# Kernel tuning notes

Hardware: AMD Instinct MI355X
Metric: run time of the kernel (lower is better)

The kernel has to match this reference:

```python
import jax, jax.numpy as jnp
import numpy as np


def _position_table(seq_len, d_model, dtype):
    # position[i, j] = sin(i / 10000**((j+1)/d))  if j even
    #                  cos(i / 10000**((j+1)/d))  if j odd
    # (note the nonstandard (j+1)/d exponent, faithful to the source)
    i = jnp.arange(seq_len, dtype=dtype)[:, None]          # [S, 1]
    j = jnp.arange(d_model, dtype=dtype)[None, :]          # [1, D]
    pf = i / jnp.power(jnp.asarray(10000.0, dtype), (j + 1.0) / d_model)  # [S, D]
    even = (jnp.arange(d_model) % 2 == 0)[None, :]
    return jnp.where(even, jnp.sin(pf), jnp.cos(pf))       # [S, D]


def setup_inputs() -> dict:
    key = jax.random.key(0)
    x = jax.random.normal(key, (4, 8192, 1024), dtype=jnp.float32)
    return {"x": x}


def reference(x) -> jnp.ndarray:
    B, S, D = x.shape
    pos = _position_table(S, D, x.dtype)
    return x + pos[None, :, :]
```

## Files before the change

### kernel.cpp

```cpp
#include <hip/hip_runtime.h>
#include <math.h>

#define PE_S 8192
#define PE_D 1024
#define PE_B 4

__global__ __launch_bounds__(256) void position_encoder_kernel(
    const float* __restrict__ x, float* __restrict__ out) {
    const int tid = blockIdx.x * blockDim.x + threadIdx.x;
    const int d4  = tid & (PE_D / 4 - 1);
    const int s   = tid >> 8;
    const int d0  = d4 << 2;

    const float fs = (float)s;
    const float a2 = -0.012976281620653760f;
    const float w0 = exp2f((float)(d0 + 1) * a2);
    const float w1 = exp2f((float)(d0 + 2) * a2);
    const float w2 = exp2f((float)(d0 + 3) * a2);
    const float w3 = exp2f((float)(d0 + 4) * a2);

    float4 p;
    p.x = sinf(fs * w0);
    p.y = cosf(fs * w1);
    p.z = sinf(fs * w2);
    p.w = cosf(fs * w3);

    const size_t base  = (size_t)s * PE_D + (size_t)d0;
    const size_t plane = (size_t)PE_S * PE_D;
#pragma unroll
    for (int b = 0; b < PE_B; ++b) {
        const float4 v = *reinterpret_cast<const float4*>(x + (size_t)b * plane + base);
        float4 o;
        o.x = v.x + p.x;
        o.y = v.y + p.y;
        o.z = v.z + p.z;
        o.w = v.w + p.w;
        *reinterpret_cast<float4*>(out + (size_t)b * plane + base) = o;
    }
}

extern "C" void kernel_launch(void* const* d_in, const int* in_sizes, int n_in,
                              void* d_out, int out_size, void* d_ws, size_t ws_size,
                              hipStream_t stream) {
    const float* x = (const float*)d_in[0];
    float* out = (float*)d_out;

    const int threads = 256;
    const int total_quads = PE_S * PE_D / 4;
    const int blocks = total_quads / threads;
    position_encoder_kernel<<<blocks, threads, 0, stream>>>(x, out);
}
```

Baseline: 233.1 us.

## Use hardware sin/cos with revolution-based range reduction and flatten batch loop

Replaces library sinf/cosf with AMD hardware sin/cos builtins, pre-scaling frequencies into revolutions and reducing the argument via floor plus an fma error-correction term. Each thread now processes a single float4 across the full batched tensor instead of looping over batches, which launches 4x more threads and recomputes the positional values per batch. This targets the expensive precise trig range reduction, at some accuracy risk for large arguments and with redundant transcendental work.

```diff
diff --git a/kernel.cpp b/kernel.cpp
--- a/kernel.cpp
+++ b/kernel.cpp
@@ -5,38 +5,46 @@
 #define PE_D 1024
 #define PE_B 4
 
+typedef float f32x4 __attribute__((ext_vector_type(4)));
+
+__device__ __forceinline__ float pe_sin(float fs, float wrev) {
+    float t = fs * wrev;
+    float r = t - floorf(t);
+    r += fmaf(fs, wrev, -t);
+    return __builtin_amdgcn_sinf(r);
+}
+__device__ __forceinline__ float pe_cos(float fs, float wrev) {
+    float t = fs * wrev;
+    float r = t - floorf(t);
+    r += fmaf(fs, wrev, -t);
+    return __builtin_amdgcn_cosf(r);
+}
+
 __global__ __launch_bounds__(256) void position_encoder_kernel(
     const float* __restrict__ x, float* __restrict__ out) {
     const int tid = blockIdx.x * blockDim.x + threadIdx.x;
     const int d4  = tid & (PE_D / 4 - 1);
-    const int s   = tid >> 8;
+    const int s   = (tid >> 8) & (PE_S - 1);
     const int d0  = d4 << 2;
 
     const float fs = (float)s;
-    const float a2 = -0.012976281620653760f;
-    const float w0 = exp2f((float)(d0 + 1) * a2);
-    const float w1 = exp2f((float)(d0 + 2) * a2);
-    const float w2 = exp2f((float)(d0 + 3) * a2);
-    const float w3 = exp2f((float)(d0 + 4) * a2);
+    const float A2 = -0.012976281620653760f;
+    const float C  = -2.6514961294723187f;
 
-    float4 p;
-    p.x = sinf(fs * w0);
-    p.y = cosf(fs * w1);
-    p.z = sinf(fs * w2);
-    p.w = cosf(fs * w3);
+    const float w0 = exp2f(fmaf((float)(d0 + 1), A2, C));
+    const float w1 = exp2f(fmaf((float)(d0 + 2), A2, C));
+    const float w2 = exp2f(fmaf((float)(d0 + 3), A2, C));
+    const float w3 = exp2f(fmaf((float)(d0 + 4), A2, C));
 
-    const size_t base  = (size_t)s * PE_D + (size_t)d0;
-    const size_t plane = (size_t)PE_S * PE_D;
-#pragma unroll
-    for (int b = 0; b < PE_B; ++b) {
-        const float4 v = *reinterpret_cast<const float4*>(x + (size_t)b * plane + base);
-        float4 o;
-        o.x = v.x + p.x;
-        o.y = v.y + p.y;
-        o.z = v.z + p.z;
-        o.w = v.w + p.w;
-        *reinterpret_cast<float4*>(out + (size_t)b * plane + base) = o;
-    }
+    const size_t off = (size_t)tid * 4;
+    const f32x4 v = *reinterpret_cast<const f32x4*>(x + off);
+
+    f32x4 o;
+    o.x = v.x + pe_sin(fs, w0);
+    o.y = v.y + pe_cos(fs, w1);
+    o.z = v.z + pe_sin(fs, w2);
+    o.w = v.w + pe_cos(fs, w3);
+    *reinterpret_cast<f32x4*>(out + off) = o;
 }
 
 extern "C" void kernel_launch(void* const* d_in, const int* in_sizes, int n_in,
@@ -46,7 +54,7 @@
     float* out = (float*)d_out;
 
     const int threads = 256;
-    const int total_quads = PE_S * PE_D / 4;
+    const int total_quads = PE_B * PE_S * PE_D / 4;
     const int blocks = total_quads / threads;
     position_encoder_kernel<<<blocks, threads, 0, stream>>>(x, out);
 }
```

After: 218.7 us. -6.2%, faster.
